# Kernel optimization log

Measured on AMD Instinct MI355X. Metric: run time of the kernel, lower is better.

The kernel has to match this reference:

```python
import jax, jax.numpy as jnp
import numpy as np

NUM_SAMPLES = 100


def setup_inputs() -> dict:
    key = jax.random.key(0)
    # [B, 2C, H, W]: first C channels are logits, last C are log-std
    inp = jax.random.normal(key, (8, 38, 256, 256), dtype=jnp.float32)
    return {"input": inp}


def reference(input):
    logits, log_std = jnp.split(input, 2, axis=-3)  # each [B, C, H, W]
    std = jnp.exp(log_std)
    keys = jax.random.split(jax.random.key(1), NUM_SAMPLES)

    def body(acc, k):
        eps = jax.random.normal(k, std.shape, dtype=std.dtype)
        acc = acc + jax.nn.softmax(logits + eps * std, axis=-3)
        return acc, None

    softmax_sum, _ = jax.lax.scan(body, jnp.zeros_like(logits), keys)
    return softmax_sum / NUM_SAMPLES
```

## Files before the change

kernel.cpp:

```cpp
#include <hip/hip_runtime.h>
#include <stdint.h>


#define NCH    19
#define HW     65536
#define NSAMP  100

__device__ __forceinline__ uint32_t rotl(uint32_t x, uint32_t r) {
  return __builtin_amdgcn_alignbit(x, x, 32u - r);
}

__device__ __forceinline__ void tf2x32_full(uint32_t k0, uint32_t k1,
                                            uint32_t x0, uint32_t x1,
                                            uint32_t& o0, uint32_t& o1) {
  const uint32_t k2 = k0 ^ k1 ^ 0x1BD11BDAu;
#define TFR(r) { x0 += x1; x1 = rotl(x1, r) ^ x0; }
  x0 += k0; x1 += k1;
  TFR(13u) TFR(15u) TFR(26u) TFR(6u)
  x0 += k1; x1 += k2 + 1u;
  TFR(17u) TFR(29u) TFR(16u) TFR(24u)
  x0 += k2; x1 += k0 + 2u;
  TFR(13u) TFR(15u) TFR(26u) TFR(6u)
  x0 += k0; x1 += k1 + 3u;
  TFR(17u) TFR(29u) TFR(16u) TFR(24u)
  x0 += k1; x1 += k2 + 4u;
  TFR(13u) TFR(15u) TFR(26u) TFR(6u)
  x0 += k2; x1 += k0 + 5u;
#undef TFR
  o0 = x0; o1 = x1;
}

__device__ __forceinline__ uint32_t tf_fold(uint32_t k0, uint32_t k1, uint32_t k2,
                                            uint32_t x1in) {
  uint32_t x0, x1;
  x1 = x1in + k1;
  x0 = k0 + x1;
  x1 = rotl(x1, 13u) ^ x0;
  x0 += x1; x1 = rotl(x1, 15u) ^ x0;
  x0 += x1; x1 = rotl(x1, 26u) ^ x0;
  x0 += x1; x1 = rotl(x1,  6u) ^ x0;
  x1 += k2 + 1u;
  x0 = x0 + k1 + x1; x1 = rotl(x1, 17u) ^ x0;
  x0 += x1; x1 = rotl(x1, 29u) ^ x0;
  x0 += x1; x1 = rotl(x1, 16u) ^ x0;
  x0 += x1; x1 = rotl(x1, 24u) ^ x0;
  x1 += k0 + 2u;
  x0 = x0 + k2 + x1; x1 = rotl(x1, 13u) ^ x0;
  x0 += x1; x1 = rotl(x1, 15u) ^ x0;
  x0 += x1; x1 = rotl(x1, 26u) ^ x0;
  x0 += x1; x1 = rotl(x1,  6u) ^ x0;
  x1 += k1 + 3u;
  x0 = x0 + k0 + x1; x1 = rotl(x1, 17u) ^ x0;
  x0 += x1; x1 = rotl(x1, 29u) ^ x0;
  x0 += x1; x1 = rotl(x1, 16u) ^ x0;
  x0 += x1; x1 = rotl(x1, 24u) ^ x0;
  x1 += k2 + 4u;
  x0 = x0 + k1 + x1; x1 = rotl(x1, 13u) ^ x0;
  x0 += x1; x1 = rotl(x1, 15u) ^ x0;
  x0 += x1; x1 = rotl(x1, 26u) ^ x0;
  x0 += x1; x1 = rotl(x1,  6u) ^ x0;
  return (x0 + k2) ^ (x1 + k0 + 5u);
}

__device__ __forceinline__ float bits_to_eps(uint32_t bits) {
  const float lo = -0.99999994f;
  float x = __uint_as_float((bits >> 9) | 0x3F800000u);
  float u = fmaf(x, 2.0f, -2.99999994f);
  u = fmaxf(u, lo);
  float t = __builtin_amdgcn_logf(fmaf(-u, u, 1.0f));
  float p;
  if (t > -7.2135401f) {
    float tw = t + 3.6067376f;
    p = 2.1176667e-09f;
    p = fmaf(p, tw, -3.7319753e-08f);
    p = fmaf(p, tw, -5.5262077e-07f);
    p = fmaf(p, tw, 9.9370361e-07f);
    p = fmaf(p, tw, 7.1355918e-05f);
    p = fmaf(p, tw, 5.9046852e-04f);
    p = fmaf(p, tw, -2.8386612e-03f);
    p = fmaf(p, tw, -2.4177230e-01f);
    p = fmaf(p, tw, 2.1233141e+00f);
  } else {
    float w = -0.69314718f * t;
    w = __fsqrt_rn(w) - 3.0f;
    p = -2.8314594e-04f;
    p = fmaf(p, w, 1.4276565e-04f);
    p = fmaf(p, w, 1.9082604e-03f);
    p = fmaf(p, w, -5.1950124e-03f);
    p = fmaf(p, w, 8.1168916e-03f);
    p = fmaf(p, w, -1.0779791e-02f);
    p = fmaf(p, w, 1.3348577e-02f);
    p = fmaf(p, w, 1.4165810e+00f);
    p = fmaf(p, w, 4.0064324e+00f);
  }
  return p * u;
}

__global__ __launch_bounds__(256, 4)
void HeteroscedasticSoftmax_kernel(const float* __restrict__ in,
                                   float* __restrict__ out) {
  __shared__ float2 sls[NCH][256];
  __shared__ uint2  skey[NSAMP];

  const int t = threadIdx.x;
  if (t < NSAMP) {
    uint32_t a, b;
    tf2x32_full(0u, 1u, 0u, (uint32_t)t, a, b);
    skey[t] = make_uint2(a, b);
  }

  const int gid = blockIdx.x * 256 + t;
  const int b_  = gid >> 16;
  const int hw  = gid & 65535;

  const float L2E = 1.4426950408889634f;
  const float* pin = in + (size_t)b_ * (2 * NCH * HW) + hw;
  float acc[NCH];
#pragma unroll
  for (int c = 0; c < NCH; ++c) {
    float lg = pin[c * HW];
    float ls = pin[(NCH + c) * HW];
    sls[c][t] = make_float2(lg * L2E, __expf(ls) * L2E);
    acc[c] = 0.0f;
  }
  __syncthreads();

  const uint32_t jbase = (uint32_t)(b_ * NCH) * (uint32_t)HW + (uint32_t)hw;

#pragma unroll 1
  for (int s = 0; s < NSAMP; ++s) {
    const uint2 kk = skey[s];
    const uint32_t k0 = __builtin_amdgcn_readfirstlane(kk.x);
    const uint32_t k1 = __builtin_amdgcn_readfirstlane(kk.y);
    const uint32_t k2 = k0 ^ k1 ^ 0x1BD11BDAu;

    float z[NCH];
#pragma unroll
    for (int c = 0; c < NCH; ++c) {
      const uint32_t bits = tf_fold(k0, k1, k2, jbase + (uint32_t)c * HW);
      const float eps = bits_to_eps(bits);
      const float2 ls = sls[c][t];
      z[c] = fmaf(eps, ls.y, ls.x);
    }

    float m0 = fmaxf(z[0], z[1]),  m1 = fmaxf(z[2], z[3]);
    float m2 = fmaxf(z[4], z[5]),  m3 = fmaxf(z[6], z[7]);
    float m4 = fmaxf(z[8], z[9]),  m5 = fmaxf(z[10], z[11]);
    float m6 = fmaxf(z[12], z[13]), m7 = fmaxf(z[14], z[15]);
    float m8 = fmaxf(z[16], z[17]);
    m0 = fmaxf(m0, m1); m2 = fmaxf(m2, m3); m4 = fmaxf(m4, m5);
    m6 = fmaxf(m6, m7); m8 = fmaxf(m8, z[18]);
    m0 = fmaxf(m0, m2); m4 = fmaxf(m4, m6);
    m0 = fmaxf(m0, m4);
    const float m = fmaxf(m0, m8);

#pragma unroll
    for (int c = 0; c < NCH; ++c) z[c] = __builtin_amdgcn_exp2f(z[c] - m);

    float s0 = z[0] + z[1],  s1 = z[2] + z[3];
    float s2 = z[4] + z[5],  s3 = z[6] + z[7];
    float s4 = z[8] + z[9],  s5 = z[10] + z[11];
    float s6 = z[12] + z[13], s7 = z[14] + z[15];
    float s8 = z[16] + z[17];
    s0 += s1; s2 += s3; s4 += s5; s6 += s7; s8 += z[18];
    s0 += s2; s4 += s6;
    s0 += s4;
    const float r = __builtin_amdgcn_rcpf(s0 + s8);

#pragma unroll
    for (int c = 0; c < NCH; ++c) acc[c] = fmaf(z[c], r, acc[c]);
  }

  float* pout = out + (size_t)b_ * (NCH * HW) + hw;
#pragma unroll
  for (int c = 0; c < NCH; ++c) pout[c * HW] = acc[c] * 0.01f;
}

extern "C" void kernel_launch(void* const* d_in, const int* in_sizes, int n_in,
                              void* d_out, int out_size, void* d_ws, size_t ws_size,
                              hipStream_t stream) {
  const float* in = (const float*)d_in[0];
  float* out = (float*)d_out;
  HeteroscedasticSoftmax_kernel<<<2048, 256, 0, stream>>>(in, out);
}
```

Baseline: 2.120 ms.

## Split each pixel's channels across four lanes with DPP softmax reductions

Each pixel is now handled by 4 lanes, each owning 5 channel slots (19 channels padded to 20). The per-sample max and sum reductions are completed with DPP lane swaps. This drops the LDS staging array and the large per-thread register arrays, and raises the launch-bounds occupancy target from 4 to 8 blocks. The intent is better latency hiding through lower register pressure and more waves. The cost is one padded slot whose random-number and inverse-error-function work is thrown away, plus extra DPP instructions on every sample.

```diff
diff --git a/kernel.cpp b/kernel.cpp
--- a/kernel.cpp
+++ b/kernel.cpp
@@ -96,11 +96,19 @@
   return p * u;
 }
 
-__global__ __launch_bounds__(256, 4)
+__device__ __forceinline__ float dpp_swap1(float v) {
+  return __int_as_float(
+      __builtin_amdgcn_mov_dpp(__float_as_int(v), 0xB1, 0xF, 0xF, true));
+}
+__device__ __forceinline__ float dpp_swap2(float v) {
+  return __int_as_float(
+      __builtin_amdgcn_mov_dpp(__float_as_int(v), 0x4E, 0xF, 0xF, true));
+}
+
+__global__ __launch_bounds__(256, 8)
 void HeteroscedasticSoftmax_kernel(const float* __restrict__ in,
                                    float* __restrict__ out) {
-  __shared__ float2 sls[NCH][256];
-  __shared__ uint2  skey[NSAMP];
+  __shared__ uint2 skey[NSAMP];
 
   const int t = threadIdx.x;
   if (t < NSAMP) {
@@ -109,23 +117,28 @@
     skey[t] = make_uint2(a, b);
   }
 
-  const int gid = blockIdx.x * 256 + t;
+  const int gid = blockIdx.x * 64 + (t >> 2);
+  const int par = t & 3;
   const int b_  = gid >> 16;
   const int hw  = gid & 65535;
 
   const float L2E = 1.4426950408889634f;
   const float* pin = in + (size_t)b_ * (2 * NCH * HW) + hw;
-  float acc[NCH];
+  float lgE[5], sdE[5], acc[5];
 #pragma unroll
-  for (int c = 0; c < NCH; ++c) {
-    float lg = pin[c * HW];
-    float ls = pin[(NCH + c) * HW];
-    sls[c][t] = make_float2(lg * L2E, __expf(ls) * L2E);
-    acc[c] = 0.0f;
+  for (int i = 0; i < 5; ++i) {
+    const int c  = 4 * i + par;
+    const int cc = (c < NCH) ? c : 0;
+    const float lg = pin[cc * HW];
+    const float ls = pin[(NCH + cc) * HW];
+    lgE[i] = (c < NCH) ? lg * L2E : -1.0e30f;
+    sdE[i] = (c < NCH) ? __expf(ls) * L2E : 0.0f;
+    acc[i] = 0.0f;
   }
   __syncthreads();
 
-  const uint32_t jbase = (uint32_t)(b_ * NCH) * (uint32_t)HW + (uint32_t)hw;
+  const uint32_t jb = (uint32_t)(b_ * NCH) * (uint32_t)HW
+                    + (uint32_t)hw + (uint32_t)(par * HW);
 
 #pragma unroll 1
   for (int s = 0; s < NSAMP; ++s) {
@@ -134,46 +147,36 @@
     const uint32_t k1 = __builtin_amdgcn_readfirstlane(kk.y);
     const uint32_t k2 = k0 ^ k1 ^ 0x1BD11BDAu;
 
-    float z[NCH];
+    float z[5];
 #pragma unroll
-    for (int c = 0; c < NCH; ++c) {
-      const uint32_t bits = tf_fold(k0, k1, k2, jbase + (uint32_t)c * HW);
+    for (int i = 0; i < 5; ++i) {
+      const uint32_t bits = tf_fold(k0, k1, k2, jb + (uint32_t)(i * 4 * HW));
       const float eps = bits_to_eps(bits);
-      const float2 ls = sls[c][t];
-      z[c] = fmaf(eps, ls.y, ls.x);
+      z[i] = fmaf(eps, sdE[i], lgE[i]);
     }
 
-    float m0 = fmaxf(z[0], z[1]),  m1 = fmaxf(z[2], z[3]);
-    float m2 = fmaxf(z[4], z[5]),  m3 = fmaxf(z[6], z[7]);
-    float m4 = fmaxf(z[8], z[9]),  m5 = fmaxf(z[10], z[11]);
-    float m6 = fmaxf(z[12], z[13]), m7 = fmaxf(z[14], z[15]);
-    float m8 = fmaxf(z[16], z[17]);
-    m0 = fmaxf(m0, m1); m2 = fmaxf(m2, m3); m4 = fmaxf(m4, m5);
-    m6 = fmaxf(m6, m7); m8 = fmaxf(m8, z[18]);
-    m0 = fmaxf(m0, m2); m4 = fmaxf(m4, m6);
-    m0 = fmaxf(m0, m4);
-    const float m = fmaxf(m0, m8);
+    float m = fmaxf(fmaxf(fmaxf(z[0], z[1]), fmaxf(z[2], z[3])), z[4]);
+    m = fmaxf(m, dpp_swap1(m));
+    m = fmaxf(m, dpp_swap2(m));
 
 #pragma unroll
-    for (int c = 0; c < NCH; ++c) z[c] = __builtin_amdgcn_exp2f(z[c] - m);
+    for (int i = 0; i < 5; ++i) z[i] = __builtin_amdgcn_exp2f(z[i] - m);
 
-    float s0 = z[0] + z[1],  s1 = z[2] + z[3];
-    float s2 = z[4] + z[5],  s3 = z[6] + z[7];
-    float s4 = z[8] + z[9],  s5 = z[10] + z[11];
-    float s6 = z[12] + z[13], s7 = z[14] + z[15];
-    float s8 = z[16] + z[17];
-    s0 += s1; s2 += s3; s4 += s5; s6 += s7; s8 += z[18];
-    s0 += s2; s4 += s6;
-    s0 += s4;
-    const float r = __builtin_amdgcn_rcpf(s0 + s8);
+    float ss = (z[0] + z[1]) + (z[2] + z[3]) + z[4];
+    ss += dpp_swap1(ss);
+    ss += dpp_swap2(ss);
+    const float r = __builtin_amdgcn_rcpf(ss);
 
 #pragma unroll
-    for (int c = 0; c < NCH; ++c) acc[c] = fmaf(z[c], r, acc[c]);
+    for (int i = 0; i < 5; ++i) acc[i] = fmaf(z[i], r, acc[i]);
   }
 
   float* pout = out + (size_t)b_ * (NCH * HW) + hw;
 #pragma unroll
-  for (int c = 0; c < NCH; ++c) pout[c * HW] = acc[c] * 0.01f;
+  for (int i = 0; i < 5; ++i) {
+    const int c = 4 * i + par;
+    if (c < NCH) pout[c * HW] = acc[i] * 0.01f;
+  }
 }
 
 extern "C" void kernel_launch(void* const* d_in, const int* in_sizes, int n_in,
@@ -181,5 +184,5 @@
                               hipStream_t stream) {
   const float* in = (const float*)d_in[0];
   float* out = (float*)d_out;
-  HeteroscedasticSoftmax_kernel<<<2048, 256, 0, stream>>>(in, out);
+  HeteroscedasticSoftmax_kernel<<<8192, 256, 0, stream>>>(in, out);
 }
```

Result: no change. 2.149 ms (+1.4%).
